# Kernel tuning notes

Hardware: AMD Instinct MI355X
Metric: run time of the kernel (lower is better)

Reference implementation:

```python
import jax, jax.numpy as jnp
import numpy as np

NU = 0.01 / np.pi  # viscosity buffer from the torch module


def _mlp(x, W_in, b_in, W_hid, b_hid, W_out, b_out):
    # x: [N, 2] -> u: [N, 1]; tanh MLP with stacked hidden layers scanned.
    h = jnp.tanh(x @ W_in + b_in)

    def step(h, wb):
        W, b = wb
        return jnp.tanh(h @ W + b), None

    h, _ = jax.lax.scan(step, h, (W_hid, b_hid))
    return h @ W_out + b_out


def setup_inputs() -> dict:
    key = jax.random.key(0)
    ks = jax.random.split(key, 10)
    N_f, N0, Nb, H, L = 131072, 4096, 2048, 128, 7
    s_in = 1.0 / np.sqrt(2.0)
    s_h = 1.0 / np.sqrt(H)
    return {
        "x_f": jax.random.normal(ks[0], (N_f, 2), jnp.float32),
        "x0_cat": jax.random.normal(ks[1], (N0, 2), jnp.float32),
        "xb_left_cat": jax.random.normal(ks[2], (Nb, 2), jnp.float32),
        "xb_right_cat": jax.random.normal(ks[3], (Nb, 2), jnp.float32),
        "W_in": jax.random.normal(ks[4], (2, H), jnp.float32) * s_in,
        "b_in": jax.random.normal(ks[5], (H,), jnp.float32) * 0.01,
        "W_hid": jax.random.normal(ks[6], (L, H, H), jnp.float32) * s_h,
        "b_hid": jax.random.normal(ks[7], (L, H), jnp.float32) * 0.01,
        "W_out": jax.random.normal(ks[8], (H, 1), jnp.float32) * s_h,
        "b_out": jax.random.normal(ks[9], (1,), jnp.float32) * 0.01,
    }


def reference(x_f, x0_cat, xb_left_cat, xb_right_cat,
              W_in, b_in, W_hid, b_hid, W_out, b_out):
    u = lambda x: _mlp(x, W_in, b_in, W_hid, b_hid, W_out, b_out)

    u_0_pred = u(x0_cat)
    u_b_left_pred = u(xb_left_cat)
    u_b_right_pred = u(xb_right_cat)

    u_f_pred = u(x_f)  # [N_f, 1]

    # Each row of u depends only on the matching row of x, so grad of the sum
    # yields per-example gradients (equivalent to torch.autograd.grad with
    # grad_outputs=ones).
    usum = lambda x: u(x).sum()
    g = jax.grad(usum)(x_f)            # [N_f, 2]
    u_x = g[:, 0:1]
    u_t = g[:, 1:2]

    # Second derivative: grad of sum(u_x) w.r.t. x, take the x-component.
    uxx_full = jax.grad(lambda x: jax.grad(usum)(x)[:, 0].sum())(x_f)
    u_xx = uxx_full[:, 0:1]

    pde_residual = u_t + u_f_pred * u_x - NU * u_xx
    return jnp.concatenate((u_0_pred, u_b_left_pred, u_b_right_pred,
                            pde_residual), axis=0)
```

## Files before the change

### kernel.cpp

```cpp
#include <hip/hip_runtime.h>
#include <math.h>

#define NU_F 0.0031830988618379067f
#define KTANH 2.885390082f

typedef _Float16 f16x8 __attribute__((ext_vector_type(8)));
typedef float    f32x4 __attribute__((ext_vector_type(4)));

__device__ __forceinline__ float tanh_pre(float zs) {
    float e = __builtin_amdgcn_exp2f(zs);
    float r = __builtin_amdgcn_rcpf(e + 1.0f);
    return fmaf(-2.0f, r, 1.0f);
}

__device__ __forceinline__ unsigned pkf16(float a, float b) {
    auto v = __builtin_amdgcn_cvt_pkrtz(a, b);
    return __builtin_bit_cast(unsigned, v);
}

__device__ __forceinline__ void lds_barrier() {
    asm volatile("s_waitcnt lgkmcnt(0)" ::: "memory");
    __builtin_amdgcn_s_barrier();
}

__global__ void prep_wfrag(const float* __restrict__ Whid, _Float16* __restrict__ wcf)
{
    const int t    = blockIdx.x * 256 + threadIdx.x;
    const int lane = t & 63;
    const int fid  = t >> 6;
    const int ks = fid & 3;
    const int nt = (fid >> 2) & 7;
    const int l  = fid >> 5;
    const int q  = lane >> 4;
    const int nn = lane & 15;
    const int c  = ((nt >> 1) << 5) + nn * 2 + (nt & 1);
    const int k0 = ks * 32 + q * 8;
    const float* src = Whid + l * 16384 + k0 * 128 + c;
    f16x8 v;
    #pragma unroll
    for (int jj = 0; jj < 8; ++jj)
        v[jj] = (_Float16)src[jj * 128];
    *(f16x8*)(wcf + (size_t)t * 8) = v;
}

#define HR 68
#define MFMA(A, B, C) __builtin_amdgcn_mfma_f32_16x16x32_f16((A), (B), (C), 0, 0, 0)

__global__ __launch_bounds__(256, 4)
void pinn_fused(const float* __restrict__ xf,
                const float* __restrict__ x0,  const float* __restrict__ xbl,
                const float* __restrict__ xbr,
                const float* __restrict__ Win,  const float* __restrict__ bin,
                const float* __restrict__ bhid,
                const float* __restrict__ Wout, const float* __restrict__ bout,
                const _Float16* __restrict__ wcf,
                float* __restrict__ out)
{
    __shared__ unsigned Hh[2][64 * HR];
    __shared__ float xpt[128];
    __shared__ float pbuf[256];
    __shared__ float dots[64];

    const int tid  = threadIdx.x;
    const int lane = tid & 63;
    const int wv   = tid >> 6;
    const int lm   = lane & 15;
    const int lq   = lane >> 4;
    const int blk  = blockIdx.x;
    const bool isv = (blk >= 8192);

    if (!isv) {
        if (tid < 32) xpt[tid] = xf[blk * 32 + tid];
    } else {
        if (tid < 128) {
            const int vb = blk - 8192;
            const float* src = (vb < 64) ? (x0 + vb * 128)
                             : (vb < 96) ? (xbl + (vb - 64) * 128)
                                         : (xbr + (vb - 96) * 128);
            xpt[tid] = src[tid];
        }
    }

    const _Float16* pb0 = wcf + (wv * 2 + 0) * 2048 + lane * 8;
    const _Float16* pb1 = wcf + (wv * 2 + 1) * 2048 + lane * 8;
    const float* bptr = bhid + wv * 32 + lm * 2;
    f16x8 cB0 = *(const f16x8*)pb0;
    f16x8 cB1 = *(const f16x8*)pb1;
    float2 btc = *(const float2*)bptr;

    __syncthreads();

    const int cp = tid & 63;
    {
        const float2 w01 = *(const float2*)&Win[cp * 2];
        const float2 w11 = *(const float2*)&Win[128 + cp * 2];
        const float2 bb  = *(const float2*)&bin[cp * 2];
        const float w01sx = w01.x * KTANH, w01sy = w01.y * KTANH;
        const float w11sx = w11.x * KTANH, w11sy = w11.y * KTANH;
        const float bbsx  = bb.x  * KTANH, bbsy  = bb.y  * KTANH;
        if (!isv) {
            const int p0 = wv * 4;
            #pragma unroll
            for (int i = 0; i < 4; ++i) {
                const int p = p0 + i;
                const float x = xpt[2 * p], tt = xpt[2 * p + 1];
                const float ya = tanh_pre(fmaf(x, w01sx, fmaf(tt, w11sx, bbsx)));
                const float yb = tanh_pre(fmaf(x, w01sy, fmaf(tt, w11sy, bbsy)));
                const float da = 1.f - ya * ya, db = 1.f - yb * yb;
                Hh[0][(0 * 16 + p) * HR + cp] = pkf16(ya, yb);
                Hh[0][(1 * 16 + p) * HR + cp] = pkf16(da * w01.x, db * w01.y);
                Hh[0][(2 * 16 + p) * HR + cp] = pkf16(da * w11.x, db * w11.y);
                Hh[0][(3 * 16 + p) * HR + cp] =
                    pkf16(-2.f * ya * da * w01.x * w01.x,
                          -2.f * yb * db * w01.y * w01.y);
            }
        } else {
            const int p0 = wv * 16;
            #pragma unroll
            for (int i = 0; i < 16; ++i) {
                const int p = p0 + i;
                const float x = xpt[2 * p], tt = xpt[2 * p + 1];
                const float ya = tanh_pre(fmaf(x, w01sx, fmaf(tt, w11sx, bbsx)));
                const float yb = tanh_pre(fmaf(x, w01sy, fmaf(tt, w11sy, bbsy)));
                Hh[0][p * HR + cp] = pkf16(ya, yb);
            }
        }
    }
    lds_barrier();

    const int wc = wv * 16 + lm;

    if (!isv) {
        for (int l = 0; l < 7; ++l) {
            const unsigned* Hc = Hh[l & 1];
            unsigned*       Hn = Hh[(l & 1) ^ 1];
            const float bbs0 = btc.x * KTANH, bbs1 = btc.y * KTANH;

            f32x4 acc[4][2];
            #pragma unroll
            for (int s = 0; s < 4; ++s)
                #pragma unroll
                for (int j = 0; j < 2; ++j) acc[s][j] = (f32x4){0.f, 0.f, 0.f, 0.f};

            {
                const int ro = lq * 4;
                const f16x8 ah0 = *(const f16x8*)&Hc[(0 * 16 + lm) * HR + ro];
                const f16x8 ah1 = *(const f16x8*)&Hc[(1 * 16 + lm) * HR + ro];
                const f16x8 ah2 = *(const f16x8*)&Hc[(2 * 16 + lm) * HR + ro];
                const f16x8 ah3 = *(const f16x8*)&Hc[(3 * 16 + lm) * HR + ro];
                acc[0][0] = MFMA(ah0, cB0, acc[0][0]);
                acc[1][0] = MFMA(ah1, cB0, acc[1][0]);
                acc[2][0] = MFMA(ah2, cB0, acc[2][0]);
                acc[3][0] = MFMA(ah3, cB0, acc[3][0]);
                acc[0][1] = MFMA(ah0, cB1, acc[0][1]);
                acc[1][1] = MFMA(ah1, cB1, acc[1][1]);
                acc[2][1] = MFMA(ah2, cB1, acc[2][1]);
                acc[3][1] = MFMA(ah3, cB1, acc[3][1]);
            }
            #pragma unroll
            for (int ks = 1; ks < 4; ++ks) {
                const int ro = ks * 16 + lq * 4;
                const f16x8 ah0 = *(const f16x8*)&Hc[(0 * 16 + lm) * HR + ro];
                const f16x8 ah1 = *(const f16x8*)&Hc[(1 * 16 + lm) * HR + ro];
                const f16x8 ah2 = *(const f16x8*)&Hc[(2 * 16 + lm) * HR + ro];
                const f16x8 ah3 = *(const f16x8*)&Hc[(3 * 16 + lm) * HR + ro];
                const f16x8 b0 = *(const f16x8*)(pb0 + ks * 512);
                const f16x8 b1 = *(const f16x8*)(pb1 + ks * 512);
                acc[0][0] = MFMA(ah0, b0, acc[0][0]);
                acc[1][0] = MFMA(ah1, b0, acc[1][0]);
                acc[2][0] = MFMA(ah2, b0, acc[2][0]);
                acc[3][0] = MFMA(ah3, b0, acc[3][0]);
                acc[0][1] = MFMA(ah0, b1, acc[0][1]);
                acc[1][1] = MFMA(ah1, b1, acc[1][1]);
                acc[2][1] = MFMA(ah2, b1, acc[2][1]);
                acc[3][1] = MFMA(ah3, b1, acc[3][1]);
            }

            pb0 += 16384; pb1 += 16384;
            if (l < 6) {
                cB0 = *(const f16x8*)pb0;
                cB1 = *(const f16x8*)pb1;
                btc = *(const float2*)(bptr + 128);
                bptr += 128;
            }

            #pragma unroll
            for (int r = 0; r < 4; ++r) {
                const int p = lq * 4 + r;
                float h[2][4];
                #pragma unroll
                for (int j = 0; j < 2; ++j) {
                    const float zx  = acc[1][j][r];
                    const float zt  = acc[2][j][r];
                    const float zxx = acc[3][j][r];
                    const float y = tanh_pre(fmaf(acc[0][j][r], KTANH,
                                                  j ? bbs1 : bbs0));
                    const float d = fmaf(-y, y, 1.f);
                    const float m = d * zx;
                    h[j][0] = y;
                    h[j][1] = m;
                    h[j][2] = d * zt;
                    h[j][3] = fmaf(d, zxx, -2.f * (y * m) * zx);
                }
                #pragma unroll
                for (int s = 0; s < 4; ++s)
                    Hn[(s * 16 + p) * HR + wc] = pkf16(h[0][s], h[1][s]);
            }
            lds_barrier();
        }
    } else {
        for (int l = 0; l < 7; ++l) {
            const unsigned* Hc = Hh[l & 1];
            unsigned*       Hn = Hh[(l & 1) ^ 1];
            const float bbs0 = btc.x * KTANH, bbs1 = btc.y * KTANH;

            f32x4 acc[4][2];
            #pragma unroll
            for (int mt = 0; mt < 4; ++mt)
                #pragma unroll
                for (int j = 0; j < 2; ++j) acc[mt][j] = (f32x4){0.f, 0.f, 0.f, 0.f};

            {
                const int ro = lq * 4;
                f16x8 ah[4];
                #pragma unroll
                for (int mt = 0; mt < 4; ++mt)
                    ah[mt] = *(const f16x8*)&Hc[(mt * 16 + lm) * HR + ro];
                #pragma unroll
                for (int mt = 0; mt < 4; ++mt) {
                    acc[mt][0] = MFMA(ah[mt], cB0, acc[mt][0]);
                    acc[mt][1] = MFMA(ah[mt], cB1, acc[mt][1]);
                }
            }
            #pragma unroll
            for (int ks = 1; ks < 4; ++ks) {
                const int ro = ks * 16 + lq * 4;
                f16x8 ah[4];
                #pragma unroll
                for (int mt = 0; mt < 4; ++mt)
                    ah[mt] = *(const f16x8*)&Hc[(mt * 16 + lm) * HR + ro];
                const f16x8 b0 = *(const f16x8*)(pb0 + ks * 512);
                const f16x8 b1 = *(const f16x8*)(pb1 + ks * 512);
                #pragma unroll
                for (int mt = 0; mt < 4; ++mt) {
                    acc[mt][0] = MFMA(ah[mt], b0, acc[mt][0]);
                    acc[mt][1] = MFMA(ah[mt], b1, acc[mt][1]);
                }
            }

            pb0 += 16384; pb1 += 16384;
            if (l < 6) {
                cB0 = *(const f16x8*)pb0;
                cB1 = *(const f16x8*)pb1;
                btc = *(const float2*)(bptr + 128);
                bptr += 128;
            }

            #pragma unroll
            for (int mt = 0; mt < 4; ++mt) {
                #pragma unroll
                for (int r = 0; r < 4; ++r) {
                    const int p = mt * 16 + lq * 4 + r;
                    const float y0 = tanh_pre(fmaf(acc[mt][0][r], KTANH, bbs0));
                    const float y1 = tanh_pre(fmaf(acc[mt][1][r], KTANH, bbs1));
                    Hn[p * HR + wc] = pkf16(y0, y1);
                }
            }
            lds_barrier();
        }
    }

    {
        const int st = lane;
        const int cb = wv * 16;
        float part = 0.f;
        #pragma unroll
        for (int c8 = 0; c8 < 4; ++c8) {
            const f16x8 hv = *(const f16x8*)&Hh[1][st * HR + cb + c8 * 4];
            const float4 w1 = *(const float4*)&Wout[wv * 32 + c8 * 8];
            const float4 w2 = *(const float4*)&Wout[wv * 32 + c8 * 8 + 4];
            part = fmaf((float)hv[0], w1.x, part);
            part = fmaf((float)hv[1], w1.y, part);
            part = fmaf((float)hv[2], w1.z, part);
            part = fmaf((float)hv[3], w1.w, part);
            part = fmaf((float)hv[4], w2.x, part);
            part = fmaf((float)hv[5], w2.y, part);
            part = fmaf((float)hv[6], w2.z, part);
            part = fmaf((float)hv[7], w2.w, part);
        }
        pbuf[wv * 64 + st] = part;
    }
    lds_barrier();
    if (tid < 64)
        dots[tid] = (pbuf[tid] + pbuf[64 + tid]) + (pbuf[128 + tid] + pbuf[192 + tid]);
    lds_barrier();
    if (!isv) {
        if (tid < 16) {
            const float u = dots[tid] + bout[0];
            out[8192 + blk * 16 + tid] =
                dots[32 + tid] + u * dots[16 + tid] - NU_F * dots[48 + tid];
        }
    } else {
        if (tid < 64) out[(blk - 8192) * 64 + tid] = dots[tid] + bout[0];
    }
}

extern "C" void kernel_launch(void* const* d_in, const int* in_sizes, int n_in,
                              void* d_out, int out_size, void* d_ws, size_t ws_size,
                              hipStream_t stream) {
    (void)in_sizes; (void)n_in; (void)ws_size; (void)out_size;
    const float* xf   = (const float*)d_in[0];
    const float* x0   = (const float*)d_in[1];
    const float* xbl  = (const float*)d_in[2];
    const float* xbr  = (const float*)d_in[3];
    const float* Win  = (const float*)d_in[4];
    const float* bin  = (const float*)d_in[5];
    const float* Whid = (const float*)d_in[6];
    const float* bhid = (const float*)d_in[7];
    const float* Wout = (const float*)d_in[8];
    const float* bout = (const float*)d_in[9];
    float* out = (float*)d_out;

    _Float16* wcf = (_Float16*)d_ws;

    hipLaunchKernelGGL(prep_wfrag, dim3(14336 / 256), dim3(256), 0, stream,
                       Whid, wcf);
    hipLaunchKernelGGL(pinn_fused, dim3(8192 + 128), dim3(256), 0, stream,
                       xf, x0, xbl, xbr, Win, bin, bhid, Wout, bout, wcf, out);
}
```

Measured before the change: 214.9 us.

## Process two point groups per block and interleave their MFMA and epilogue phases

Each block now handles two independent tiles of points, with one held in each LDS buffer. The layer loop alternates between them so that the tanh and derivative epilogue of one tile can overlap the MFMA k-loop of the other. This halves the grid and loads each weight fragment once for two tiles. The cost is a second set of accumulators, which raises register pressure under launch_bounds(256,4), and a more complex barrier schedule.

```diff
diff --git a/kernel.cpp b/kernel.cpp
--- a/kernel.cpp
+++ b/kernel.cpp
@@ -46,6 +46,92 @@
 #define HR 68
 #define MFMA(A, B, C) __builtin_amdgcn_mfma_f32_16x16x32_f16((A), (B), (C), 0, 0, 0)
 
+__device__ __forceinline__ void kloop(f32x4 (&acc)[4][2],
+        const unsigned* __restrict__ Hc,
+        const f16x8& cB0, const f16x8& cB1,
+        const _Float16* __restrict__ pb0, const _Float16* __restrict__ pb1,
+        int lm, int lq)
+{
+    #pragma unroll
+    for (int s = 0; s < 4; ++s)
+        #pragma unroll
+        for (int j = 0; j < 2; ++j) acc[s][j] = (f32x4){0.f, 0.f, 0.f, 0.f};
+    {
+        const int ro = lq * 4;
+        const f16x8 ah0 = *(const f16x8*)&Hc[(0 * 16 + lm) * HR + ro];
+        const f16x8 ah1 = *(const f16x8*)&Hc[(1 * 16 + lm) * HR + ro];
+        const f16x8 ah2 = *(const f16x8*)&Hc[(2 * 16 + lm) * HR + ro];
+        const f16x8 ah3 = *(const f16x8*)&Hc[(3 * 16 + lm) * HR + ro];
+        acc[0][0] = MFMA(ah0, cB0, acc[0][0]);
+        acc[1][0] = MFMA(ah1, cB0, acc[1][0]);
+        acc[2][0] = MFMA(ah2, cB0, acc[2][0]);
+        acc[3][0] = MFMA(ah3, cB0, acc[3][0]);
+        acc[0][1] = MFMA(ah0, cB1, acc[0][1]);
+        acc[1][1] = MFMA(ah1, cB1, acc[1][1]);
+        acc[2][1] = MFMA(ah2, cB1, acc[2][1]);
+        acc[3][1] = MFMA(ah3, cB1, acc[3][1]);
+    }
+    #pragma unroll
+    for (int ks = 1; ks < 4; ++ks) {
+        const int ro = ks * 16 + lq * 4;
+        const f16x8 ah0 = *(const f16x8*)&Hc[(0 * 16 + lm) * HR + ro];
+        const f16x8 ah1 = *(const f16x8*)&Hc[(1 * 16 + lm) * HR + ro];
+        const f16x8 ah2 = *(const f16x8*)&Hc[(2 * 16 + lm) * HR + ro];
+        const f16x8 ah3 = *(const f16x8*)&Hc[(3 * 16 + lm) * HR + ro];
+        const f16x8 b0 = *(const f16x8*)(pb0 + ks * 512);
+        const f16x8 b1 = *(const f16x8*)(pb1 + ks * 512);
+        acc[0][0] = MFMA(ah0, b0, acc[0][0]);
+        acc[1][0] = MFMA(ah1, b0, acc[1][0]);
+        acc[2][0] = MFMA(ah2, b0, acc[2][0]);
+        acc[3][0] = MFMA(ah3, b0, acc[3][0]);
+        acc[0][1] = MFMA(ah0, b1, acc[0][1]);
+        acc[1][1] = MFMA(ah1, b1, acc[1][1]);
+        acc[2][1] = MFMA(ah2, b1, acc[2][1]);
+        acc[3][1] = MFMA(ah3, b1, acc[3][1]);
+    }
+}
+
+__device__ __forceinline__ void epi_deriv(const f32x4 (&acc)[4][2],
+        float bbs0, float bbs1, unsigned* __restrict__ Hn, int lq, int wc)
+{
+    #pragma unroll
+    for (int r = 0; r < 4; ++r) {
+        const int p = lq * 4 + r;
+        float h[2][4];
+        #pragma unroll
+        for (int j = 0; j < 2; ++j) {
+            const float zx  = acc[1][j][r];
+            const float zt  = acc[2][j][r];
+            const float zxx = acc[3][j][r];
+            const float y = tanh_pre(fmaf(acc[0][j][r], KTANH, j ? bbs1 : bbs0));
+            const float d = fmaf(-y, y, 1.f);
+            const float m = d * zx;
+            h[j][0] = y;
+            h[j][1] = m;
+            h[j][2] = d * zt;
+            h[j][3] = fmaf(d, zxx, -2.f * (y * m) * zx);
+        }
+        #pragma unroll
+        for (int s = 0; s < 4; ++s)
+            Hn[(s * 16 + p) * HR + wc] = pkf16(h[0][s], h[1][s]);
+    }
+}
+
+__device__ __forceinline__ void epi_val(const f32x4 (&acc)[4][2],
+        float bbs0, float bbs1, unsigned* __restrict__ Hn, int lq, int wc)
+{
+    #pragma unroll
+    for (int mt = 0; mt < 4; ++mt) {
+        #pragma unroll
+        for (int r = 0; r < 4; ++r) {
+            const int p = mt * 16 + lq * 4 + r;
+            const float y0 = tanh_pre(fmaf(acc[mt][0][r], KTANH, bbs0));
+            const float y1 = tanh_pre(fmaf(acc[mt][1][r], KTANH, bbs1));
+            Hn[p * HR + wc] = pkf16(y0, y1);
+        }
+    }
+}
+
 __global__ __launch_bounds__(256, 4)
 void pinn_fused(const float* __restrict__ xf,
                 const float* __restrict__ x0,  const float* __restrict__ xbl,
@@ -57,9 +143,9 @@
                 float* __restrict__ out)
 {
     __shared__ unsigned Hh[2][64 * HR];
-    __shared__ float xpt[128];
-    __shared__ float pbuf[256];
-    __shared__ float dots[64];
+    __shared__ float xpt[256];
+    __shared__ float pbuf[512];
+    __shared__ float dots[128];
 
     const int tid  = threadIdx.x;
     const int lane = tid & 63;
@@ -67,18 +153,17 @@
     const int lm   = lane & 15;
     const int lq   = lane >> 4;
     const int blk  = blockIdx.x;
-    const bool isv = (blk >= 8192);
+    const bool isv = (blk >= 4096);
 
     if (!isv) {
-        if (tid < 32) xpt[tid] = xf[blk * 32 + tid];
+        if (tid < 64) xpt[tid] = xf[blk * 64 + tid];
     } else {
-        if (tid < 128) {
-            const int vb = blk - 8192;
-            const float* src = (vb < 64) ? (x0 + vb * 128)
-                             : (vb < 96) ? (xbl + (vb - 64) * 128)
-                                         : (xbr + (vb - 96) * 128);
-            xpt[tid] = src[tid];
-        }
+        const int vb = blk - 4096;
+        const int vp = vb * 2 + (tid >> 7);
+        const float* src = (vp < 64) ? (x0 + vp * 128)
+                         : (vp < 96) ? (xbl + (vp - 64) * 128)
+                                     : (xbr + (vp - 96) * 128);
+        xpt[tid] = src[tid & 127];
     }
 
     const _Float16* pb0 = wcf + (wv * 2 + 0) * 2048 + lane * 8;
@@ -86,7 +171,8 @@
     const float* bptr = bhid + wv * 32 + lm * 2;
     f16x8 cB0 = *(const f16x8*)pb0;
     f16x8 cB1 = *(const f16x8*)pb1;
-    float2 btc = *(const float2*)bptr;
+    float2 btc_cur = *(const float2*)bptr;
+    float2 btc_prev;
 
     __syncthreads();
 
@@ -99,209 +185,147 @@
         const float w11sx = w11.x * KTANH, w11sy = w11.y * KTANH;
         const float bbsx  = bb.x  * KTANH, bbsy  = bb.y  * KTANH;
         if (!isv) {
-            const int p0 = wv * 4;
             #pragma unroll
-            for (int i = 0; i < 4; ++i) {
-                const int p = p0 + i;
-                const float x = xpt[2 * p], tt = xpt[2 * p + 1];
-                const float ya = tanh_pre(fmaf(x, w01sx, fmaf(tt, w11sx, bbsx)));
-                const float yb = tanh_pre(fmaf(x, w01sy, fmaf(tt, w11sy, bbsy)));
-                const float da = 1.f - ya * ya, db = 1.f - yb * yb;
-                Hh[0][(0 * 16 + p) * HR + cp] = pkf16(ya, yb);
-                Hh[0][(1 * 16 + p) * HR + cp] = pkf16(da * w01.x, db * w01.y);
-                Hh[0][(2 * 16 + p) * HR + cp] = pkf16(da * w11.x, db * w11.y);
-                Hh[0][(3 * 16 + p) * HR + cp] =
-                    pkf16(-2.f * ya * da * w01.x * w01.x,
-                          -2.f * yb * db * w01.y * w01.y);
+            for (int g = 0; g < 2; ++g) {
+                const int xo = g * 32;
+                const int p0 = wv * 4;
+                #pragma unroll
+                for (int i = 0; i < 4; ++i) {
+                    const int p = p0 + i;
+                    const float x = xpt[xo + 2 * p], tt = xpt[xo + 2 * p + 1];
+                    const float ya = tanh_pre(fmaf(x, w01sx, fmaf(tt, w11sx, bbsx)));
+                    const float yb = tanh_pre(fmaf(x, w01sy, fmaf(tt, w11sy, bbsy)));
+                    const float da = 1.f - ya * ya, db = 1.f - yb * yb;
+                    unsigned* H = Hh[g];
+                    H[(0 * 16 + p) * HR + cp] = pkf16(ya, yb);
+                    H[(1 * 16 + p) * HR + cp] = pkf16(da * w01.x, db * w01.y);
+                    H[(2 * 16 + p) * HR + cp] = pkf16(da * w11.x, db * w11.y);
+                    H[(3 * 16 + p) * HR + cp] =
+                        pkf16(-2.f * ya * da * w01.x * w01.x,
+                              -2.f * yb * db * w01.y * w01.y);
+                }
             }
         } else {
-            const int p0 = wv * 16;
             #pragma unroll
-            for (int i = 0; i < 16; ++i) {
-                const int p = p0 + i;
-                const float x = xpt[2 * p], tt = xpt[2 * p + 1];
-                const float ya = tanh_pre(fmaf(x, w01sx, fmaf(tt, w11sx, bbsx)));
-                const float yb = tanh_pre(fmaf(x, w01sy, fmaf(tt, w11sy, bbsy)));
-                Hh[0][p * HR + cp] = pkf16(ya, yb);
+            for (int g = 0; g < 2; ++g) {
+                const int xo = g * 128;
+                const int p0 = wv * 16;
+                #pragma unroll
+                for (int i = 0; i < 16; ++i) {
+                    const int p = p0 + i;
+                    const float x = xpt[xo + 2 * p], tt = xpt[xo + 2 * p + 1];
+                    const float ya = tanh_pre(fmaf(x, w01sx, fmaf(tt, w11sx, bbsx)));
+                    const float yb = tanh_pre(fmaf(x, w01sy, fmaf(tt, w11sy, bbsy)));
+                    Hh[g][p * HR + cp] = pkf16(ya, yb);
+                }
             }
         }
     }
     lds_barrier();
 
     const int wc = wv * 16 + lm;
+
+    f32x4 accA[4][2], accB[4][2];
 
     if (!isv) {
         for (int l = 0; l < 7; ++l) {
-            const unsigned* Hc = Hh[l & 1];
-            unsigned*       Hn = Hh[(l & 1) ^ 1];
-            const float bbs0 = btc.x * KTANH, bbs1 = btc.y * KTANH;
-
-            f32x4 acc[4][2];
-            #pragma unroll
-            for (int s = 0; s < 4; ++s)
-                #pragma unroll
-                for (int j = 0; j < 2; ++j) acc[s][j] = (f32x4){0.f, 0.f, 0.f, 0.f};
-
-            {
-                const int ro = lq * 4;
-                const f16x8 ah0 = *(const f16x8*)&Hc[(0 * 16 + lm) * HR + ro];
-                const f16x8 ah1 = *(const f16x8*)&Hc[(1 * 16 + lm) * HR + ro];
-                const f16x8 ah2 = *(const f16x8*)&Hc[(2 * 16 + lm) * HR + ro];
-                const f16x8 ah3 = *(const f16x8*)&Hc[(3 * 16 + lm) * HR + ro];
-                acc[0][0] = MFMA(ah0, cB0, acc[0][0]);
-                acc[1][0] = MFMA(ah1, cB0, acc[1][0]);
-                acc[2][0] = MFMA(ah2, cB0, acc[2][0]);
-                acc[3][0] = MFMA(ah3, cB0, acc[3][0]);
-                acc[0][1] = MFMA(ah0, cB1, acc[0][1]);
-                acc[1][1] = MFMA(ah1, cB1, acc[1][1]);
-                acc[2][1] = MFMA(ah2, cB1, acc[2][1]);
-                acc[3][1] = MFMA(ah3, cB1, acc[3][1]);
-            }
-            #pragma unroll
-            for (int ks = 1; ks < 4; ++ks) {
-                const int ro = ks * 16 + lq * 4;
-                const f16x8 ah0 = *(const f16x8*)&Hc[(0 * 16 + lm) * HR + ro];
-                const f16x8 ah1 = *(const f16x8*)&Hc[(1 * 16 + lm) * HR + ro];
-                const f16x8 ah2 = *(const f16x8*)&Hc[(2 * 16 + lm) * HR + ro];
-                const f16x8 ah3 = *(const f16x8*)&Hc[(3 * 16 + lm) * HR + ro];
-                const f16x8 b0 = *(const f16x8*)(pb0 + ks * 512);
-                const f16x8 b1 = *(const f16x8*)(pb1 + ks * 512);
-                acc[0][0] = MFMA(ah0, b0, acc[0][0]);
-                acc[1][0] = MFMA(ah1, b0, acc[1][0]);
-                acc[2][0] = MFMA(ah2, b0, acc[2][0]);
-                acc[3][0] = MFMA(ah3, b0, acc[3][0]);
-                acc[0][1] = MFMA(ah0, b1, acc[0][1]);
-                acc[1][1] = MFMA(ah1, b1, acc[1][1]);
-                acc[2][1] = MFMA(ah2, b1, acc[2][1]);
-                acc[3][1] = MFMA(ah3, b1, acc[3][1]);
-            }
-
+            kloop(accA, Hh[0], cB0, cB1, pb0, pb1, lm, lq);
+            if (l > 0)
+                epi_deriv(accB, btc_prev.x * KTANH, btc_prev.y * KTANH,
+                          Hh[1], lq, wc);
+            lds_barrier();
+
+            kloop(accB, Hh[1], cB0, cB1, pb0, pb1, lm, lq);
+            btc_prev = btc_cur;
             pb0 += 16384; pb1 += 16384;
             if (l < 6) {
                 cB0 = *(const f16x8*)pb0;
                 cB1 = *(const f16x8*)pb1;
-                btc = *(const float2*)(bptr + 128);
+                btc_cur = *(const float2*)(bptr + 128);
                 bptr += 128;
             }
-
-            #pragma unroll
-            for (int r = 0; r < 4; ++r) {
-                const int p = lq * 4 + r;
-                float h[2][4];
-                #pragma unroll
-                for (int j = 0; j < 2; ++j) {
-                    const float zx  = acc[1][j][r];
-                    const float zt  = acc[2][j][r];
-                    const float zxx = acc[3][j][r];
-                    const float y = tanh_pre(fmaf(acc[0][j][r], KTANH,
-                                                  j ? bbs1 : bbs0));
-                    const float d = fmaf(-y, y, 1.f);
-                    const float m = d * zx;
-                    h[j][0] = y;
-                    h[j][1] = m;
-                    h[j][2] = d * zt;
-                    h[j][3] = fmaf(d, zxx, -2.f * (y * m) * zx);
-                }
-                #pragma unroll
-                for (int s = 0; s < 4; ++s)
-                    Hn[(s * 16 + p) * HR + wc] = pkf16(h[0][s], h[1][s]);
-            }
+            epi_deriv(accA, btc_prev.x * KTANH, btc_prev.y * KTANH,
+                      Hh[0], lq, wc);
             lds_barrier();
         }
+        epi_deriv(accB, btc_prev.x * KTANH, btc_prev.y * KTANH, Hh[1], lq, wc);
+        lds_barrier();
     } else {
         for (int l = 0; l < 7; ++l) {
-            const unsigned* Hc = Hh[l & 1];
-            unsigned*       Hn = Hh[(l & 1) ^ 1];
-            const float bbs0 = btc.x * KTANH, bbs1 = btc.y * KTANH;
-
-            f32x4 acc[4][2];
-            #pragma unroll
-            for (int mt = 0; mt < 4; ++mt)
-                #pragma unroll
-                for (int j = 0; j < 2; ++j) acc[mt][j] = (f32x4){0.f, 0.f, 0.f, 0.f};
-
-            {
-                const int ro = lq * 4;
-                f16x8 ah[4];
-                #pragma unroll
-                for (int mt = 0; mt < 4; ++mt)
-                    ah[mt] = *(const f16x8*)&Hc[(mt * 16 + lm) * HR + ro];
-                #pragma unroll
-                for (int mt = 0; mt < 4; ++mt) {
-                    acc[mt][0] = MFMA(ah[mt], cB0, acc[mt][0]);
-                    acc[mt][1] = MFMA(ah[mt], cB1, acc[mt][1]);
-                }
-            }
-            #pragma unroll
-            for (int ks = 1; ks < 4; ++ks) {
-                const int ro = ks * 16 + lq * 4;
-                f16x8 ah[4];
-                #pragma unroll
-                for (int mt = 0; mt < 4; ++mt)
-                    ah[mt] = *(const f16x8*)&Hc[(mt * 16 + lm) * HR + ro];
-                const f16x8 b0 = *(const f16x8*)(pb0 + ks * 512);
-                const f16x8 b1 = *(const f16x8*)(pb1 + ks * 512);
-                #pragma unroll
-                for (int mt = 0; mt < 4; ++mt) {
-                    acc[mt][0] = MFMA(ah[mt], b0, acc[mt][0]);
-                    acc[mt][1] = MFMA(ah[mt], b1, acc[mt][1]);
-                }
-            }
-
+            kloop(accA, Hh[0], cB0, cB1, pb0, pb1, lm, lq);
+            if (l > 0)
+                epi_val(accB, btc_prev.x * KTANH, btc_prev.y * KTANH,
+                        Hh[1], lq, wc);
+            lds_barrier();
+
+            kloop(accB, Hh[1], cB0, cB1, pb0, pb1, lm, lq);
+            btc_prev = btc_cur;
             pb0 += 16384; pb1 += 16384;
             if (l < 6) {
                 cB0 = *(const f16x8*)pb0;
                 cB1 = *(const f16x8*)pb1;
-                btc = *(const float2*)(bptr + 128);
+                btc_cur = *(const float2*)(bptr + 128);
                 bptr += 128;
             }
-
-            #pragma unroll
-            for (int mt = 0; mt < 4; ++mt) {
-                #pragma unroll
-                for (int r = 0; r < 4; ++r) {
-                    const int p = mt * 16 + lq * 4 + r;
-                    const float y0 = tanh_pre(fmaf(acc[mt][0][r], KTANH, bbs0));
-                    const float y1 = tanh_pre(fmaf(acc[mt][1][r], KTANH, bbs1));
-                    Hn[p * HR + wc] = pkf16(y0, y1);
-                }
-            }
+            epi_val(accA, btc_prev.x * KTANH, btc_prev.y * KTANH, Hh[0], lq, wc);
             lds_barrier();
         }
+        epi_val(accB, btc_prev.x * KTANH, btc_prev.y * KTANH, Hh[1], lq, wc);
+        lds_barrier();
     }
 
     {
         const int st = lane;
         const int cb = wv * 16;
-        float part = 0.f;
+        float pA = 0.f, pB = 0.f;
         #pragma unroll
         for (int c8 = 0; c8 < 4; ++c8) {
-            const f16x8 hv = *(const f16x8*)&Hh[1][st * HR + cb + c8 * 4];
+            const f16x8 hA = *(const f16x8*)&Hh[0][st * HR + cb + c8 * 4];
+            const f16x8 hB = *(const f16x8*)&Hh[1][st * HR + cb + c8 * 4];
             const float4 w1 = *(const float4*)&Wout[wv * 32 + c8 * 8];
             const float4 w2 = *(const float4*)&Wout[wv * 32 + c8 * 8 + 4];
-            part = fmaf((float)hv[0], w1.x, part);
-            part = fmaf((float)hv[1], w1.y, part);
-            part = fmaf((float)hv[2], w1.z, part);
-            part = fmaf((float)hv[3], w1.w, part);
-            part = fmaf((float)hv[4], w2.x, part);
-            part = fmaf((float)hv[5], w2.y, part);
-            part = fmaf((float)hv[6], w2.z, part);
-            part = fmaf((float)hv[7], w2.w, part);
-        }
-        pbuf[wv * 64 + st] = part;
+            pA = fmaf((float)hA[0], w1.x, pA);
+            pA = fmaf((float)hA[1], w1.y, pA);
+            pA = fmaf((float)hA[2], w1.z, pA);
+            pA = fmaf((float)hA[3], w1.w, pA);
+            pA = fmaf((float)hA[4], w2.x, pA);
+            pA = fmaf((float)hA[5], w2.y, pA);
+            pA = fmaf((float)hA[6], w2.z, pA);
+            pA = fmaf((float)hA[7], w2.w, pA);
+            pB = fmaf((float)hB[0], w1.x, pB);
+            pB = fmaf((float)hB[1], w1.y, pB);
+            pB = fmaf((float)hB[2], w1.z, pB);
+            pB = fmaf((float)hB[3], w1.w, pB);
+            pB = fmaf((float)hB[4], w2.x, pB);
+            pB = fmaf((float)hB[5], w2.y, pB);
+            pB = fmaf((float)hB[6], w2.z, pB);
+            pB = fmaf((float)hB[7], w2.w, pB);
+        }
+        pbuf[wv * 64 + st] = pA;
+        pbuf[256 + wv * 64 + st] = pB;
     }
     lds_barrier();
-    if (tid < 64)
-        dots[tid] = (pbuf[tid] + pbuf[64 + tid]) + (pbuf[128 + tid] + pbuf[192 + tid]);
+    if (tid < 128) {
+        const float* q = pbuf + (tid >> 6) * 256;
+        const int t = tid & 63;
+        dots[tid] = (q[t] + q[64 + t]) + (q[128 + t] + q[192 + t]);
+    }
     lds_barrier();
     if (!isv) {
         if (tid < 16) {
             const float u = dots[tid] + bout[0];
-            out[8192 + blk * 16 + tid] =
+            out[8192 + blk * 32 + tid] =
                 dots[32 + tid] + u * dots[16 + tid] - NU_F * dots[48 + tid];
+        } else if (tid >= 64 && tid < 80) {
+            const int t = tid - 64;
+            const float u = dots[64 + t] + bout[0];
+            out[8192 + blk * 32 + 16 + t] =
+                dots[96 + t] + u * dots[80 + t] - NU_F * dots[112 + t];
         }
     } else {
-        if (tid < 64) out[(blk - 8192) * 64 + tid] = dots[tid] + bout[0];
+        const int vb = blk - 4096;
+        if (tid < 128)
+            out[vb * 128 + tid] = dots[tid] + bout[0];
     }
 }
 
@@ -325,6 +349,6 @@
 
     hipLaunchKernelGGL(prep_wfrag, dim3(14336 / 256), dim3(256), 0, stream,
                        Whid, wcf);
-    hipLaunchKernelGGL(pinn_fused, dim3(8192 + 128), dim3(256), 0, stream,
+    hipLaunchKernelGGL(pinn_fused, dim3(4096 + 64), dim3(256), 0, stream,
                        xf, x0, xbl, xbr, Win, bin, bhid, Wout, bout, wcf, out);
 }
```

Measured after the change: 227.9 us. +6.1%, slower.
